# Kernel optimization log

Hardware: AMD Instinct MI355X
Metric: run time of the kernel (lower is better)

The kernel has to match this reference:

```python
import jax, jax.numpy as jnp
import numpy as np

B, S, E, FEAT, ATT, NCLS, VOCAB = 32, 512, 512, 256, 10, 8, 32000
# NOTE: original code requires S == E (attentive_content [S,S] assigned into a [S,E] buffer)


def setup_inputs() -> dict:
    key = jax.random.key(0)
    ks = jax.random.split(key, 8)
    x = jax.random.randint(ks[0], (B, S), 0, VOCAB)
    emb = jax.random.normal(ks[1], (VOCAB, E), dtype=jnp.float32) * 0.02
    A = jax.random.uniform(ks[2], (E, ATT), dtype=jnp.float32, minval=-0.1, maxval=0.1)
    Wh = jax.random.normal(ks[3], (FEAT, E, 3), dtype=jnp.float32) * 0.02   # h_conv, k=3, no bias
    Wc = jax.random.normal(ks[4], (FEAT, E), dtype=jnp.float32) * 0.02      # c_conv, k=1, no bias
    tanh_bias = jnp.zeros((FEAT,), dtype=jnp.float32)
    Wfc = jax.random.normal(ks[5], (NCLS, FEAT), dtype=jnp.float32) * 0.02
    bfc = jnp.zeros((NCLS,), dtype=jnp.float32)
    return {"x": x, "emb": emb, "A": A, "Wh": Wh, "Wc": Wc,
            "tanh_bias": tanh_bias, "Wfc": Wfc, "bfc": bfc}


def reference(x, emb, A, Wh, Wc, tanh_bias, Wfc, bfc):
    ex = emb[x]                                    # [B,S,E] embedding lookup
    # batched version of the per-sample loop: mm -> softmax -> mm
    scores = jnp.einsum('bse,ea->bsa', ex, A)      # [B,S,ATT]
    attn = jax.nn.softmax(scores, axis=-1)         # softmax over attention dim (2D default)
    att = jnp.einsum('bsa,bta->bst', attn, scores)  # [B,S,S]  (S == E)
    # h branch: conv1d(k=3, valid) over time, then global max-pool
    h = jax.lax.conv_general_dilated(ex.transpose(0, 2, 1), Wh, (1,), 'VALID',
                                     dimension_numbers=('NCH', 'OIH', 'NCH'))  # [B,F,S-2]
    h = jnp.max(h, axis=-1)                        # [B,F]
    # c branch: k=1 conv over att (permuted), i.e. channel mix, then global max-pool
    c = jnp.max(jnp.einsum('blc,fc->bfl', att, Wc), axis=-1)  # [B,F]
    out = jnp.tanh(h + c + tanh_bias)
    return out @ Wfc.T + bfc                       # [B,num_class]
```

## Files before the change

### kernel.cpp

```cpp
#include <hip/hip_runtime.h>
#include <math.h>

#define B 32
#define S 512
#define E 512
#define FEAT 256
#define ATT 10
#define NCLS 8

using short8 = __attribute__((ext_vector_type(8))) short;
using f32x4  = __attribute__((ext_vector_type(4))) float;

__device__ __forceinline__ unsigned short f2bf(float f) {
    unsigned int u = __float_as_uint(f);
    return (unsigned short)((u + 0x7fffu + ((u >> 16) & 1u)) >> 16);
}

__device__ __forceinline__ void gl16(const void* g, void* l) {
    __builtin_amdgcn_global_load_lds(
        (const __attribute__((address_space(1))) unsigned int*)g,
        (__attribute__((address_space(3))) unsigned int*)l, 16, 0, 0);
}

__global__ __launch_bounds__(256) void k_front(
        const int* __restrict__ x, const float* __restrict__ emb,
        const float* __restrict__ A, const float* __restrict__ Wh,
        const float* __restrict__ bfc, unsigned short* __restrict__ ex16,
        unsigned short* __restrict__ Whk16,
        float* __restrict__ sc12, float* __restrict__ at12,
        float* __restrict__ out) {
    const int blk = blockIdx.x;
    const int tid = threadIdx.x;
    if (blk < 2048) {
        const int wave = tid >> 6, lane = tid & 63;
        f32x4 av4[20];
        const f32x4* ap4 = (const f32x4*)(A + (size_t)lane * 80);
#pragma unroll
        for (int q = 0; q < 20; ++q) av4[q] = ap4[q];
#pragma unroll
        for (int rep = 0; rep < 2; ++rep) {
            const int bs = blk * 8 + wave * 2 + rep;
            const int row = x[bs];
            const f32x4* src = (const f32x4*)(emb + (size_t)row * E);
            const f32x4 v0 = src[lane * 2], v1 = src[lane * 2 + 1];
            float v[8] = {v0[0], v0[1], v0[2], v0[3], v1[0], v1[1], v1[2], v1[3]};

            short8 sv;
#pragma unroll
            for (int j = 0; j < 8; ++j) sv[j] = (short)f2bf(v[j]);
            *(short8*)(ex16 + (size_t)bs * E + lane * 8) = sv;

            float acc[ATT] = {};
#pragma unroll
            for (int j = 0; j < 8; ++j)
#pragma unroll
                for (int a = 0; a < ATT; ++a) {
                    const int idx = j * ATT + a;
                    acc[a] = fmaf(v[j], av4[idx >> 2][idx & 3], acc[a]);
                }
#pragma unroll
            for (int a = 0; a < ATT; ++a)
#pragma unroll
                for (int off = 1; off < 64; off <<= 1) acc[a] += __shfl_xor(acc[a], off);

            if (lane == 0) {
                float m = -1e30f;
#pragma unroll
                for (int a = 0; a < ATT; ++a) m = fmaxf(m, acc[a]);
                float ev[ATT], sum = 0.f;
#pragma unroll
                for (int a = 0; a < ATT; ++a) { ev[a] = expf(acc[a] - m); sum += ev[a]; }
                const float inv = 1.f / sum;
                float* sp = sc12 + (size_t)bs * 12;
                float* tp = at12 + (size_t)bs * 12;
                *(f32x4*)(sp)     = (f32x4){acc[0], acc[1], acc[2], acc[3]};
                *(f32x4*)(sp + 4) = (f32x4){acc[4], acc[5], acc[6], acc[7]};
                *(f32x4*)(sp + 8) = (f32x4){acc[8], acc[9], 0.f, 0.f};
                *(f32x4*)(tp)     = (f32x4){ev[0] * inv, ev[1] * inv, ev[2] * inv, ev[3] * inv};
                *(f32x4*)(tp + 4) = (f32x4){ev[4] * inv, ev[5] * inv, ev[6] * inv, ev[7] * inv};
                *(f32x4*)(tp + 8) = (f32x4){ev[8] * inv, ev[9] * inv, 0.f, 0.f};
            }
        }
    } else if (blk < 2048 + FEAT) {
        const int f = blk - 2048;
        const float* src = Wh + (size_t)f * (E * 3);
        unsigned short* dst = Whk16 + (size_t)f * (E * 3);
#pragma unroll
        for (int i = 0; i < 6; ++i) {
            const int kk = tid + i * 256;
            dst[kk] = f2bf(src[(kk & 511) * 3 + (kk >> 9)]);
        }
        if (f == 0) {
            for (int i = tid; i < 2 * E; i += 256) ex16[(size_t)B * S * E + i] = 0;
        }
    } else {
        if (tid < B * NCLS) out[tid] = bfc[tid & 7];
    }
}

__global__ __launch_bounds__(512) void k_conv(const unsigned short* __restrict__ Whk,
                                              const unsigned short* __restrict__ ex16,
                                              float* __restrict__ Cpart) {
    __shared__ __align__(16) unsigned short lds[2][32768];
    const int b = blockIdx.x;
    const int fbase = blockIdx.y * 128;
    const int lbase = blockIdx.z * 128;
    const int tid = threadIdx.x;
    const int wave = tid >> 6, lane = tid & 63;
    const int g = wave >> 2;
    const int sub = wave & 3;
    const int wm = sub >> 1, wn = sub & 1;
    const int lane15 = lane & 15, g4 = lane >> 4;
    const int tg = sub * 64 + lane;
    const int rr = tg >> 3, slot = tg & 7;
    const unsigned short* exb = ex16 + (size_t)b * S * E;

    f32x4 acc[4][4];
#pragma unroll
    for (int mf = 0; mf < 4; ++mf)
#pragma unroll
        for (int nf = 0; nf < 4; ++nf) acc[mf][nf] = (f32x4){0.f, 0.f, 0.f, 0.f};

    auto stage = [&](int t, unsigned short* buf) {
        const int kkg = g * 768 + (t << 6);
        const int tap = kkg >> 9;
        const int e0  = kkg & 511;
        unsigned short* la = buf + g * 16384;
        unsigned short* lb = la + 8192;
#pragma unroll
        for (int i = 0; i < 4; ++i) {
            const int r = i * 32 + rr;
            gl16(Whk + (size_t)(fbase + r) * 1536 + kkg + ((slot ^ (r & 7)) << 3),
                 la + i * 2048 + sub * 512);
            gl16(exb + (size_t)(lbase + r + tap) * E + e0 + ((slot ^ (r & 7)) << 3),
                 lb + i * 2048 + sub * 512);
        }
    };

    auto compute = [&](const unsigned short* buf) {
        const char* la = (const char*)(buf + g * 16384);
        const char* lb = la + 16384;
#pragma unroll
        for (int kh = 0; kh < 2; ++kh) {
            short8 av[4], bv[4];
#pragma unroll
            for (int mf = 0; mf < 4; ++mf) {
                const int row = wm * 64 + mf * 16 + lane15;
                av[mf] = *(const short8*)(la + row * 128 +
                                          ((((kh << 2) | g4) ^ (row & 7)) << 4));
            }
#pragma unroll
            for (int nf = 0; nf < 4; ++nf) {
                const int row = wn * 64 + nf * 16 + lane15;
                bv[nf] = *(const short8*)(lb + row * 128 +
                                          ((((kh << 2) | g4) ^ (row & 7)) << 4));
            }
#pragma unroll
            for (int mf = 0; mf < 4; ++mf)
#pragma unroll
                for (int nf = 0; nf < 4; ++nf)
                    acc[mf][nf] = __builtin_amdgcn_mfma_f32_16x16x32_bf16(
                        av[mf], bv[nf], acc[mf][nf], 0, 0, 0);
        }
    };

    stage(0, lds[0]);
    asm volatile("s_waitcnt vmcnt(0)" ::: "memory");
    __builtin_amdgcn_s_barrier();

    for (int t = 0; t < 12; ++t) {
        if (t + 1 < 12) stage(t + 1, lds[(t + 1) & 1]);
        compute(lds[t & 1]);
        if (t + 1 < 12) {
            asm volatile("s_waitcnt vmcnt(0)" ::: "memory");
            __builtin_amdgcn_s_barrier();
        }
    }

    __syncthreads();
    f32x4* lf = (f32x4*)&lds[0][0];
    if (g == 1) {
#pragma unroll
        for (int mf = 0; mf < 4; ++mf)
#pragma unroll
            for (int nf = 0; nf < 4; ++nf)
                lf[(mf * 4 + nf) * 256 + sub * 64 + lane] = acc[mf][nf];
    }
    __syncthreads();
    if (g == 0) {
#pragma unroll
        for (int mf = 0; mf < 4; ++mf)
#pragma unroll
            for (int nf = 0; nf < 4; ++nf)
                acc[mf][nf] += lf[(mf * 4 + nf) * 256 + sub * 64 + lane];

#pragma unroll
        for (int mf = 0; mf < 4; ++mf) {
#pragma unroll
            for (int j = 0; j < 4; ++j) {
                float m = -1e30f;
#pragma unroll
                for (int nf = 0; nf < 4; ++nf) {
                    const int l = lbase + wn * 64 + nf * 16 + lane15;
                    if (l < S - 2) m = fmaxf(m, acc[mf][nf][j]);
                }
#pragma unroll
                for (int off = 1; off < 16; off <<= 1) m = fmaxf(m, __shfl_xor(m, off));
                if (lane15 == 0) {
                    const int f = fbase + wm * 64 + mf * 16 + g4 * 4 + j;
                    Cpart[(((size_t)b * FEAT + f) << 3) + blockIdx.z * 2 + wn] = m;
                }
            }
        }
    }
}

__global__ __launch_bounds__(256) void k_chc(
        const float* __restrict__ sc12, const float* __restrict__ at12,
        const float* __restrict__ Wc, const float* __restrict__ Cpart,
        const float* __restrict__ tb, const float* __restrict__ Wfc,
        float* __restrict__ out) {
    const int fg = blockIdx.x, b = blockIdx.y;
    const int tid = threadIdx.x;
    const int wave = tid >> 6, lane = tid & 63;
    const int f0 = fg * 32 + wave * 8;
    __shared__ float shc[32];
    __shared__ float ps[256];

    f32x4 wc[8][2];
#pragma unroll
    for (int ff = 0; ff < 8; ++ff) {
        const float* wp = Wc + (size_t)(f0 + ff) * E + lane * 8;
        wc[ff][0] = *(const f32x4*)wp;
        wc[ff][1] = *(const f32x4*)(wp + 4);
    }

    f32x4 g[8][3];
#pragma unroll
    for (int ff = 0; ff < 8; ++ff)
#pragma unroll
        for (int q = 0; q < 3; ++q) g[ff][q] = (f32x4){0.f, 0.f, 0.f, 0.f};

    const f32x4* scp = (const f32x4*)(sc12 + (size_t)b * S * 12);
#pragma unroll
    for (int j = 0; j < 8; ++j) {
        const int t = lane * 8 + j;
        const f32x4 s0 = scp[t * 3], s1 = scp[t * 3 + 1], s2 = scp[t * 3 + 2];
#pragma unroll
        for (int ff = 0; ff < 8; ++ff) {
            const float w = wc[ff][j >> 2][j & 3];
            g[ff][0] += s0 * w; g[ff][1] += s1 * w; g[ff][2] += s2 * w;
        }
    }
#pragma unroll
    for (int ff = 0; ff < 8; ++ff)
#pragma unroll
        for (int q = 0; q < 3; ++q)
#pragma unroll
            for (int c = 0; c < 4; ++c)
#pragma unroll
                for (int off = 1; off < 64; off <<= 1)
                    g[ff][q][c] += __shfl_xor(g[ff][q][c], off);

    const f32x4* atp = (const f32x4*)(at12 + (size_t)b * S * 12);
    float mc[8];
#pragma unroll
    for (int ff = 0; ff < 8; ++ff) mc[ff] = -1e30f;
#pragma unroll
    for (int j = 0; j < 8; ++j) {
        const int t = lane * 8 + j;
        const f32x4 a0 = atp[t * 3], a1 = atp[t * 3 + 1], a2 = atp[t * 3 + 2];
#pragma unroll
        for (int ff = 0; ff < 8; ++ff) {
            const f32x4 p = a0 * g[ff][0] + a1 * g[ff][1] + a2 * g[ff][2];
            mc[ff] = fmaxf(mc[ff], p[0] + p[1] + p[2] + p[3]);
        }
    }
#pragma unroll
    for (int ff = 0; ff < 8; ++ff)
#pragma unroll
        for (int off = 1; off < 64; off <<= 1)
            mc[ff] = fmaxf(mc[ff], __shfl_xor(mc[ff], off));

    if (lane == 0) {
#pragma unroll
        for (int ff = 0; ff < 8; ++ff) {
            const int f = f0 + ff;
            const float* cp = Cpart + (((size_t)b * FEAT + f) << 3);
            float mh = cp[0];
#pragma unroll
            for (int q = 1; q < 8; ++q) mh = fmaxf(mh, cp[q]);
            shc[wave * 8 + ff] = tanhf(mh + mc[ff] + tb[f]);
        }
    }
    __syncthreads();

    const int n = tid & 7, fl = tid >> 3;
    ps[tid] = shc[fl] * Wfc[(size_t)n * FEAT + fg * 32 + fl];
    __syncthreads();
    if (tid < 8) {
        float s = 0.f;
#pragma unroll
        for (int q = 0; q < 32; ++q) s += ps[tid + 8 * q];
        atomicAdd(&out[b * NCLS + tid], s);
    }
}

extern "C" void kernel_launch(void* const* d_in, const int* in_sizes, int n_in,
                              void* d_out, int out_size, void* d_ws, size_t ws_size,
                              hipStream_t stream) {
    const int* x      = (const int*)d_in[0];
    const float* emb  = (const float*)d_in[1];
    const float* A    = (const float*)d_in[2];
    const float* Wh   = (const float*)d_in[3];
    const float* Wc   = (const float*)d_in[4];
    const float* tb   = (const float*)d_in[5];
    const float* Wfc  = (const float*)d_in[6];
    const float* bfc  = (const float*)d_in[7];
    float* out = (float*)d_out;

    unsigned short* ex16  = (unsigned short*)d_ws;
    unsigned short* Whk16 = ex16 + (size_t)B * S * E + 2 * E;
    float* sc12 = (float*)(Whk16 + (size_t)FEAT * 3 * E);
    float* at12 = sc12 + (size_t)B * S * 12;
    float* Cpart = at12 + (size_t)B * S * 12;

    k_front<<<2048 + FEAT + 1, 256, 0, stream>>>(x, emb, A, Wh, bfc,
                                                 ex16, Whk16, sc12, at12, out);
    k_conv<<<dim3(B, 2, 4), 512, 0, stream>>>(Whk16, ex16, Cpart);
    k_chc<<<dim3(8, B), 256, 0, stream>>>(sc12, at12, Wc, Cpart, tb, Wfc, out);
}
```

Before: 62.74 us.

## Load conv weight fragments directly from global into registers, bypassing LDS

```diff
diff --git a/kernel.cpp b/kernel.cpp
--- a/kernel.cpp
+++ b/kernel.cpp
@@ -101,7 +101,7 @@
 __global__ __launch_bounds__(512) void k_conv(const unsigned short* __restrict__ Whk,
                                               const unsigned short* __restrict__ ex16,
                                               float* __restrict__ Cpart) {
-    __shared__ __align__(16) unsigned short lds[2][32768];
+    __shared__ __align__(16) unsigned short lds[2][16384];
     const int b = blockIdx.x;
     const int fbase = blockIdx.y * 128;
     const int lbase = blockIdx.z * 128;
@@ -114,6 +114,8 @@
     const int tg = sub * 64 + lane;
     const int rr = tg >> 3, slot = tg & 7;
     const unsigned short* exb = ex16 + (size_t)b * S * E;
+    const unsigned short* WA =
+        Whk + (size_t)(fbase + wm * 64 + lane15) * 1536 + g * 768 + g4 * 8;
 
     f32x4 acc[4][4];
 #pragma unroll
@@ -125,30 +127,28 @@
         const int kkg = g * 768 + (t << 6);
         const int tap = kkg >> 9;
         const int e0  = kkg & 511;
-        unsigned short* la = buf + g * 16384;
-        unsigned short* lb = la + 8192;
+        unsigned short* lb = buf + g * 8192;
 #pragma unroll
         for (int i = 0; i < 4; ++i) {
             const int r = i * 32 + rr;
-            gl16(Whk + (size_t)(fbase + r) * 1536 + kkg + ((slot ^ (r & 7)) << 3),
-                 la + i * 2048 + sub * 512);
             gl16(exb + (size_t)(lbase + r + tap) * E + e0 + ((slot ^ (r & 7)) << 3),
                  lb + i * 2048 + sub * 512);
         }
     };
 
-    auto compute = [&](const unsigned short* buf) {
-        const char* la = (const char*)(buf + g * 16384);
-        const char* lb = la + 16384;
+    auto loadA = [&](int t, short8 (&av)[2][4]) {
+#pragma unroll
+        for (int kh = 0; kh < 2; ++kh)
+#pragma unroll
+            for (int mf = 0; mf < 4; ++mf)
+                av[kh][mf] = *(const short8*)(WA + mf * 16 * 1536 + (t << 6) + kh * 32);
+    };
+
+    auto compute = [&](const unsigned short* buf, const short8 (&av)[2][4]) {
+        const char* lb = (const char*)(buf + g * 8192);
 #pragma unroll
         for (int kh = 0; kh < 2; ++kh) {
-            short8 av[4], bv[4];
-#pragma unroll
-            for (int mf = 0; mf < 4; ++mf) {
-                const int row = wm * 64 + mf * 16 + lane15;
-                av[mf] = *(const short8*)(la + row * 128 +
-                                          ((((kh << 2) | g4) ^ (row & 7)) << 4));
-            }
+            short8 bv[4];
 #pragma unroll
             for (int nf = 0; nf < 4; ++nf) {
                 const int row = wn * 64 + nf * 16 + lane15;
@@ -160,18 +160,25 @@
 #pragma unroll
                 for (int nf = 0; nf < 4; ++nf)
                     acc[mf][nf] = __builtin_amdgcn_mfma_f32_16x16x32_bf16(
-                        av[mf], bv[nf], acc[mf][nf], 0, 0, 0);
+                        av[kh][mf], bv[nf], acc[mf][nf], 0, 0, 0);
         }
     };
 
+    short8 avA[2][4], avB[2][4];
     stage(0, lds[0]);
+    loadA(0, avA);
     asm volatile("s_waitcnt vmcnt(0)" ::: "memory");
     __builtin_amdgcn_s_barrier();
 
-    for (int t = 0; t < 12; ++t) {
-        if (t + 1 < 12) stage(t + 1, lds[(t + 1) & 1]);
-        compute(lds[t & 1]);
-        if (t + 1 < 12) {
+    for (int t = 0; t < 12; t += 2) {
+        stage(t + 1, lds[1]);
+        loadA(t + 1, avB);
+        compute(lds[0], avA);
+        asm volatile("s_waitcnt vmcnt(0)" ::: "memory");
+        __builtin_amdgcn_s_barrier();
+        if (t + 2 < 12) { stage(t + 2, lds[0]); loadA(t + 2, avA); }
+        compute(lds[1], avB);
+        if (t + 2 < 12) {
             asm volatile("s_waitcnt vmcnt(0)" ::: "memory");
             __builtin_amdgcn_s_barrier();
         }
```

After: 78.54 us. 25.2% more time.
